# Kernel tuning notes

Hardware: AMD Instinct MI355X
Metric: run time of the kernel (lower is better)

The kernel has to match this reference:

```python
import jax, jax.numpy as jnp
import numpy as np

NUM_TOKENS = 4096
HIDDEN = 2048
INTER = 1408
NUM_EXPERTS = 8
TOP_K = 2


def setup_inputs() -> dict:
    key = jax.random.key(0)
    k1, k2, k3, k4, k5 = jax.random.split(key, 5)
    hidden_states = jax.random.normal(k1, (NUM_TOKENS, HIDDEN), dtype=jnp.float32)
    # w1: (E, 2*I, H) gate+up fused; w2: (E, H, I)
    w1 = jax.random.normal(k2, (NUM_EXPERTS, 2 * INTER, HIDDEN), dtype=jnp.float32) * (1.0 / np.sqrt(HIDDEN))
    w2 = jax.random.normal(k3, (NUM_EXPERTS, HIDDEN, INTER), dtype=jnp.float32) * (1.0 / np.sqrt(INTER))
    raw = jax.random.uniform(k4, (NUM_TOKENS, TOP_K), dtype=jnp.float32)
    topk_weights = raw / jnp.sum(raw, axis=-1, keepdims=True)  # router softmax-normalized weights
    topk_ids = jax.random.randint(k5, (NUM_TOKENS, TOP_K), 0, NUM_EXPERTS, dtype=jnp.int32)
    return {"hidden_states": hidden_states, "w1": w1, "w2": w2,
            "topk_weights": topk_weights, "topk_ids": topk_ids}


def reference(hidden_states, w1, w2, topk_weights, topk_ids):
    """Math-equivalent of fused_experts (dispatch -> grouped gate_up GEMM ->
    SwiGLU -> grouped down GEMM -> weighted scatter-combine).

    Expressed densely per expert (E is small and fixed), which yields the
    identical output to the sorted/grouped-GEMM formulation.
    """
    E = w1.shape[0]
    inter = w1.shape[1] // 2
    dtype = hidden_states.dtype
    # gate_up projection for every expert: [E, N, 2I]
    gate_up = jnp.einsum('nh,eih->eni', hidden_states, w1)
    gate, up = gate_up[..., :inter], gate_up[..., inter:]
    act = jax.nn.silu(gate) * up  # npu_swiglu: silu(first half) * second half
    # down projection: [E, N, H]
    expert_out = jnp.einsum('eni,ehi->enh', act, w2)
    # combine weight per (token, expert): sum of topk_weights where routed
    one_hot = jax.nn.one_hot(topk_ids, E, dtype=dtype)          # [N, K, E]
    combine = jnp.sum(topk_weights[:, :, None] * one_hot, axis=1)  # [N, E]
    return jnp.einsum('ne,enh->nh', combine, expert_out)
```

## Files before the change

kernel.cpp:

```cpp
#include <hip/hip_runtime.h>
#include <hip/hip_bf16.h>

#define NTOK 4096
#define HID 2048
#define INTER 1408
#define NEXP 8
#define NPAIR 8192
#define NKT1 32
#define NK2 44
#define G2SZ 24576

typedef short bf16x8 __attribute__((ext_vector_type(8)));
typedef float f32x4 __attribute__((ext_vector_type(4)));

__device__ __forceinline__ unsigned short f2bf(float f) {
  unsigned u = __builtin_bit_cast(unsigned, f);
  u += 0x7fffu + ((u >> 16) & 1u);
  return (unsigned short)(u >> 16);
}
__device__ __forceinline__ float bf2f(unsigned short v) {
  return __builtin_bit_cast(float, (unsigned)v << 16);
}

__device__ __forceinline__ void gload16(const void* g, void* l) {
  __builtin_amdgcn_global_load_lds(
      (const __attribute__((address_space(1))) void*)g,
      (__attribute__((address_space(3))) void*)l, 16, 0, 0);
}

__device__ __forceinline__ int xcd_swz(int lin, int nwg) {
  int xcd = lin & 7, base = lin >> 3;
  int q = nwg >> 3, r = nwg & 7;
  return (xcd < r ? xcd * (q + 1) : r * (q + 1) + (xcd - r) * q) + base;
}

#define BAR __builtin_amdgcn_s_barrier()
#define SCHED0 __builtin_amdgcn_sched_barrier(0)
#define LGKM0 asm volatile("s_waitcnt lgkmcnt(0)" ::: "memory")
#define VM6 asm volatile("s_waitcnt vmcnt(6)" ::: "memory")
#define VM3 asm volatile("s_waitcnt vmcnt(3)" ::: "memory")
#define VM0 asm volatile("s_waitcnt vmcnt(0)" ::: "memory")
#define PRIO1 __builtin_amdgcn_s_setprio(1)
#define PRIO0 __builtin_amdgcn_s_setprio(0)

__global__ void k_prep(const float* __restrict__ hs, const float* __restrict__ w1,
                       unsigned short* __restrict__ dst,
                       const int* __restrict__ ids, int* __restrict__ ctrl,
                       unsigned short* __restrict__ row_token,
                       unsigned short* __restrict__ inv_row) {
  if (blockIdx.x == 0) {
    __shared__ int cnt[NEXP], cur[NEXP];
    int t = threadIdx.x;
    if (t < NEXP) cnt[t] = 0;
    __syncthreads();
    for (int p = t; p < NPAIR; p += 512) atomicAdd(&cnt[ids[p]], 1);
    __syncthreads();
    if (t == 0) {
      int acc = 0, T1 = 0, T2 = 0;
      for (int e = 0; e < NEXP; ++e) {
        cur[e] = acc;
        ctrl[e] = cnt[e];
        ctrl[8 + e] = acc;
        int n1 = (cnt[e] + 255) >> 8;
        for (int m = 0; m < n1; ++m) { ctrl[32 + T1] = e; ctrl[72 + T1] = m; ++T1; }
        int n2 = (cnt[e] + 127) >> 7;
        for (int m = 0; m < n2; ++m) { ctrl[112 + T2] = e; ctrl[184 + T2] = m; ++T2; }
        acc += cnt[e];
      }
      ctrl[16] = T1;
      ctrl[17] = T2;
    }
    __syncthreads();
    for (int p = t; p < NPAIR; p += 512) {
      int e = ids[p];
      int pos = atomicAdd(&cur[e], 1);
      row_token[pos] = (unsigned short)(p >> 1);
      inv_row[p] = (unsigned short)pos;
    }
    return;
  }
  const int N0 = NTOK * HID / 4;
  const int N1 = N0 + NEXP * 2 * INTER * HID / 4;
  int stride = (gridDim.x - 1) * 512;
  for (int i = (blockIdx.x - 1) * 512 + threadIdx.x; i < N1; i += stride) {
    const float* s = (i < N0) ? hs : w1;
    int o = (i < N0) ? i : i - N0;
    float4 v = reinterpret_cast<const float4*>(s)[o];
    ushort4 u;
    u.x = f2bf(v.x); u.y = f2bf(v.y); u.z = f2bf(v.z); u.w = f2bf(v.w);
    reinterpret_cast<ushort4*>(dst)[i] = u;
  }
}


#define G1_STAGE_A(BB, u, ktile) \
  gload16(asrc[(u)*2+0] + (ktile)*64, lds + (BB) + ((u)*2+0)*4096 + wvb); \
  gload16(asrc[(u)*2+1] + (ktile)*64, lds + (BB) + ((u)*2+1)*4096 + wvb);
#define G1_STAGE_B(BB, u, ktile) \
  gload16(bsrc[(u)*2+0] + (ktile)*64, lds + (BB) + 16384 + ((u)*2+0)*4096 + wvb); \
  gload16(bsrc[(u)*2+1] + (ktile)*64, lds + (BB) + 16384 + ((u)*2+1)*4096 + wvb);

#define G1_READ_A(dst, BB, mh) \
  _Pragma("unroll") for (int m_ = 0; m_ < 4; ++m_) { \
    dst[m_][0] = *(const bf16x8*)(lds + (BB) + aoff + (mh)*8192 + m_*1024 + csw0); \
    dst[m_][1] = *(const bf16x8*)(lds + (BB) + aoff + (mh)*8192 + m_*1024 + csw1); \
  }
#define G1_READ_B(dst, BB, nh) \
  _Pragma("unroll") for (int n_ = 0; n_ < 2; ++n_) { \
    dst[n_][0] = *(const bf16x8*)(lds + (BB) + boff + (nh)*8192 + n_*1024 + csw0); \
    dst[n_][1] = *(const bf16x8*)(lds + (BB) + boff + (nh)*8192 + n_*1024 + csw1); \
  }

#define G1_MMA_Q(afr, bfr, mh, nh) \
  _Pragma("unroll") for (int m_ = 0; m_ < 4; ++m_) \
  _Pragma("unroll") for (int n_ = 0; n_ < 2; ++n_) { \
    acc[(mh)*4+m_][(nh)*2+n_] = __builtin_amdgcn_mfma_f32_16x16x32_bf16(afr[m_][0], bfr[n_][0], acc[(mh)*4+m_][(nh)*2+n_], 0, 0, 0); \
    acc[(mh)*4+m_][(nh)*2+n_] = __builtin_amdgcn_mfma_f32_16x16x32_bf16(afr[m_][1], bfr[n_][1], acc[(mh)*4+m_][(nh)*2+n_], 0, 0, 0); \
  }

#define G1_EIGHT(kt) \
  G1_READ_A(afM0, 0, 0) G1_READ_B(bfN0, 0, 0) G1_STAGE_B(32768, 1, (kt)+1); \
  BAR; LGKM0; PRIO1; G1_MMA_Q(afM0, bfN0, 0, 0) PRIO0; BAR; \
  G1_READ_B(bfN1, 0, 1) G1_STAGE_B(0, 0, (kt)+2); \
  BAR; LGKM0; PRIO1; G1_MMA_Q(afM0, bfN1, 0, 1) PRIO0; BAR; \
  G1_READ_A(afM1, 0, 1) G1_STAGE_A(0, 0, (kt)+2); \
  BAR; LGKM0; PRIO1; G1_MMA_Q(afM1, bfN1, 1, 1) PRIO0; BAR; \
  G1_STAGE_A(0, 1, (kt)+2); \
  BAR; LGKM0; PRIO1; G1_MMA_Q(afM1, bfN0, 1, 0) PRIO0; VM6; BAR; \
  G1_READ_A(afM0, 32768, 0) G1_READ_B(bfN0, 32768, 0) G1_STAGE_B(0, 1, (kt)+2); \
  BAR; LGKM0; PRIO1; G1_MMA_Q(afM0, bfN0, 0, 0) PRIO0; BAR; \
  G1_READ_B(bfN1, 32768, 1) G1_STAGE_B(32768, 0, (kt)+3); \
  BAR; LGKM0; PRIO1; G1_MMA_Q(afM0, bfN1, 0, 1) PRIO0; BAR; \
  G1_READ_A(afM1, 32768, 1) G1_STAGE_A(32768, 0, (kt)+3); \
  BAR; LGKM0; PRIO1; G1_MMA_Q(afM1, bfN1, 1, 1) PRIO0; BAR; \
  G1_STAGE_A(32768, 1, (kt)+3); \
  BAR; LGKM0; PRIO1; G1_MMA_Q(afM1, bfN0, 1, 0) PRIO0; VM6; BAR;

#define G1_EPI(kt) \
  G1_READ_A(afM0, 0, 0) G1_READ_B(bfN0, 0, 0) G1_STAGE_B(32768, 1, (kt)+1); \
  BAR; LGKM0; PRIO1; G1_MMA_Q(afM0, bfN0, 0, 0) PRIO0; BAR; \
  G1_READ_B(bfN1, 0, 1) \
  BAR; LGKM0; PRIO1; G1_MMA_Q(afM0, bfN1, 0, 1) PRIO0; BAR; \
  G1_READ_A(afM1, 0, 1) \
  BAR; LGKM0; PRIO1; G1_MMA_Q(afM1, bfN1, 1, 1) PRIO0; BAR; \
  BAR; LGKM0; PRIO1; G1_MMA_Q(afM1, bfN0, 1, 0) PRIO0; VM0; BAR; \
  G1_READ_A(afM0, 32768, 0) G1_READ_B(bfN0, 32768, 0) \
  BAR; LGKM0; PRIO1; G1_MMA_Q(afM0, bfN0, 0, 0) PRIO0; BAR; \
  G1_READ_B(bfN1, 32768, 1) \
  BAR; LGKM0; PRIO1; G1_MMA_Q(afM0, bfN1, 0, 1) PRIO0; BAR; \
  G1_READ_A(afM1, 32768, 1) \
  BAR; LGKM0; PRIO1; G1_MMA_Q(afM1, bfN1, 1, 1) PRIO0; BAR; \
  LGKM0; PRIO1; G1_MMA_Q(afM1, bfN0, 1, 0) PRIO0;

__global__ __launch_bounds__(512, 2) void k_gemm1(
    const unsigned short* __restrict__ hs,
    const unsigned short* __restrict__ w1,
    const float* __restrict__ w2f,
    unsigned short* __restrict__ w2b,
    const int* __restrict__ ctrl,
    const unsigned short* __restrict__ row_token,
    unsigned short* __restrict__ act) {
  const int T1 = ctrl[16];
  const int nwg = T1 * 11;
  const int lin = blockIdx.x;
  if (lin >= nwg) {
    const int NW2 = NEXP * HID * INTER / 4;
    int nc = gridDim.x - nwg;
    for (int i = (lin - nwg) * 512 + threadIdx.x; i < NW2; i += nc * 512) {
      float4 v = reinterpret_cast<const float4*>(w2f)[i];
      ushort4 u;
      u.x = f2bf(v.x); u.y = f2bf(v.y); u.z = f2bf(v.z); u.w = f2bf(v.w);
      reinterpret_cast<ushort4*>(w2b)[i] = u;
    }
    return;
  }
  const int wg = xcd_swz(lin, nwg);
  const int ti = wg / 11;
  const int nt = wg - ti * 11;
  const int e = ctrl[32 + ti], mt = ctrl[72 + ti];
  const int rows = ctrl[e], off_e = ctrl[8 + e];
  const int n0g = nt * 128;
  const unsigned short* w1e = w1 + (size_t)e * (2 * INTER * HID);

  __shared__ unsigned short smem[65536];
  unsigned short* lds = smem;

  const int t = threadIdx.x;
  const int lane = t & 63, wv = t >> 6;
  const int wm = wv >> 2, wn = wv & 3;
  const int lm = lane & 15, hi4 = lane >> 4;
  const int wvb = (t & 448) * 8;
  const int aoff = (wm * 64 + lm) * 64;
  const int boff = 16384 + (wn * 32 + lm) * 64;
  const int csw0 = (hi4 ^ (lm & 7)) * 8;
  const int csw1 = ((4 + hi4) ^ (lm & 7)) * 8;

  const unsigned short* asrc[4];
#pragma unroll
  for (int i = 0; i < 4; ++i) {
    int p = i * 64 + (t >> 3);
    int r = ((p >> 6) & 1) * 128 + (p >> 7) * 64 + (p & 63);
    int grow = mt * 256 + r;
    if (grow > rows - 1) grow = rows - 1;
    int token = row_token[off_e + grow];
    asrc[i] = hs + (size_t)token * HID + ((t & 7) ^ (p & 7)) * 8;
  }
  const unsigned short* bsrc[4];
#pragma unroll
  for (int i = 0; i < 4; ++i) {
    int p = i * 64 + (t >> 3);
    int nh = p >> 7, wns = (p & 127) >> 5, idx = p & 31;
    int c = n0g + wns * 32 + idx + nh * INTER;
    bsrc[i] = w1e + (size_t)c * HID + ((t & 7) ^ (p & 7)) * 8;
  }

  f32x4 acc[8][4];
#pragma unroll
  for (int i = 0; i < 8; ++i)
#pragma unroll
    for (int j = 0; j < 4; ++j) acc[i][j] = (f32x4){0.f, 0.f, 0.f, 0.f};
  bf16x8 afM0[4][2], afM1[4][2], bfN0[2][2], bfN1[2][2];

  G1_STAGE_B(0, 0, 0) G1_STAGE_A(0, 0, 0) G1_STAGE_A(0, 1, 0) G1_STAGE_B(0, 1, 0)
  G1_STAGE_B(32768, 0, 1) G1_STAGE_A(32768, 0, 1) G1_STAGE_A(32768, 1, 1)
  VM6; BAR;

  for (int kt = 0; kt + 3 < NKT1; kt += 2) { G1_EIGHT(kt) }
  G1_EPI(NKT1 - 2)

#pragma unroll
  for (int mh = 0; mh < 2; ++mh)
#pragma unroll
    for (int m = 0; m < 4; ++m)
#pragma unroll
      for (int n = 0; n < 2; ++n) {
        int col = n0g + wn * 32 + n * 16 + lm;
#pragma unroll
        for (int j = 0; j < 4; ++j) {
          int grow = mt * 256 + wm * 128 + mh * 64 + m * 16 + hi4 * 4 + j;
          if (grow < rows) {
            float g = acc[mh * 4 + m][n][j];
            float u = acc[mh * 4 + m][2 + n][j];
            float a = g / (1.0f + __expf(-g)) * u;
            act[(size_t)(off_e + grow) * INTER + col] = f2bf(a);
          }
        }
      }
}

#define T_STAGE(BB, kt) { \
  gload16(aptr + (size_t)(kt)*32, smem + (BB) + wvb16); \
  gload16(bptr0 + (size_t)(kt)*32, smem + (BB) + 8192 + wvb16); \
  gload16(bptr1 + (size_t)(kt)*32, smem + (BB) + 16384 + wvb16); }

#define T_RD(BB) { \
  _Pragma("unroll") for (int m_ = 0; m_ < 4; ++m_) \
    af[m_] = *(const bf16x8*)(smem + (BB) + arow + m_*1024 + swz); \
  _Pragma("unroll") for (int n_ = 0; n_ < 2; ++n_) { \
    b0[n_] = *(const bf16x8*)(smem + (BB) + brow + n_*1024 + swz); \
    b1[n_] = *(const bf16x8*)(smem + (BB) + brow + 8192 + n_*1024 + swz); } }

#define T_MMA \
  _Pragma("unroll") for (int m_ = 0; m_ < 4; ++m_) \
  _Pragma("unroll") for (int n_ = 0; n_ < 2; ++n_) { \
    acc0[m_][n_] = __builtin_amdgcn_mfma_f32_16x16x32_bf16(af[m_], b0[n_], acc0[m_][n_], 0, 0, 0); \
    acc1[m_][n_] = __builtin_amdgcn_mfma_f32_16x16x32_bf16(af[m_], b1[n_], acc1[m_][n_], 0, 0, 0); }

__global__ __launch_bounds__(512, 4) void k_gemm2(
    const unsigned short* __restrict__ act,
    const unsigned short* __restrict__ w2,
    const int* __restrict__ ctrl,
    unsigned short* __restrict__ eo) {
  const int T2 = ctrl[17];
  const int nwg = T2 * 8;
  const int lin = blockIdx.x;
  if (lin >= nwg) return;
  const int wg = xcd_swz(lin, nwg);
  const int ti = wg >> 3;
  const int nt = wg & 7;
  const int e = ctrl[112 + ti], mt = ctrl[184 + ti];
  const int rows = ctrl[e], off_e = ctrl[8 + e];
  const int n0 = nt * 256;
  const unsigned short* w2e = w2 + (size_t)e * (HID * INTER);

  __shared__ __align__(16) char smem[2 * G2SZ];

  const int t = threadIdx.x;
  const int lane = t & 63, wv = t >> 6;
  const int wm = wv >> 2, wn = wv & 3;
  const int lm = lane & 15, hi4 = lane >> 4;
  const int wvb16 = (t & 448) * 16;
  const int arow = wm * 4096 + lm * 64;
  const int brow = 8192 + wn * 2048 + lm * 64;
  const int swz = (hi4 ^ ((lm >> 1) & 3)) * 16;

  const unsigned short *aptr, *bptr0, *bptr1;
  {
    int cl8 = ((t & 3) ^ ((t >> 3) & 3)) * 8;
    int r = t >> 2;
    int g0 = mt * 128 + r; if (g0 > rows - 1) g0 = rows - 1;
    aptr = act + (size_t)(off_e + g0) * INTER + cl8;
    bptr0 = w2e + (size_t)(n0 + r) * INTER + cl8;
    bptr1 = w2e + (size_t)(n0 + 128 + r) * INTER + cl8;
  }

  f32x4 acc0[4][2], acc1[4][2];
#pragma unroll
  for (int m = 0; m < 4; ++m)
#pragma unroll
    for (int n = 0; n < 2; ++n) {
      acc0[m][n] = (f32x4){0.f, 0.f, 0.f, 0.f};
      acc1[m][n] = (f32x4){0.f, 0.f, 0.f, 0.f};
    }
  bf16x8 af[4], b0[2], b1[2];

  T_STAGE(0, 0)
  T_STAGE(G2SZ, 1)
  VM3; BAR;
  unsigned cur = 0, oth = G2SZ;
  for (int kt = 0; kt < NK2; ++kt) {
    T_RD(cur)
    LGKM0; BAR;
    SCHED0;
    if (kt + 2 < NK2) { T_STAGE(cur, kt + 2) }
    PRIO1; T_MMA PRIO0;
    if (kt < NK2 - 2) { VM3; BAR; }
    else if (kt == NK2 - 2) { VM0; BAR; }
    unsigned tmp = cur; cur = oth; oth = tmp;
  }

#pragma unroll
  for (int m = 0; m < 4; ++m)
#pragma unroll
    for (int n = 0; n < 2; ++n) {
      int col = n0 + wn * 32 + n * 16 + lm;
#pragma unroll
      for (int j = 0; j < 4; ++j) {
        int grow = mt * 128 + wm * 64 + m * 16 + hi4 * 4 + j;
        if (grow < rows) {
          size_t base = (size_t)(off_e + grow) * HID;
          eo[base + col] = f2bf(acc0[m][n][j]);
          eo[base + col + 128] = f2bf(acc1[m][n][j]);
        }
      }
    }
}

__global__ void k_combine(const unsigned short* __restrict__ eo,
                          const float* __restrict__ tw,
                          const unsigned short* __restrict__ inv_row,
                          float* __restrict__ out) {
  int idx = blockIdx.x * blockDim.x + threadIdx.x;
  int tok = idx >> 8;
  int c8 = (idx & 255) * 8;
  int r0 = inv_row[tok * 2], r1 = inv_row[tok * 2 + 1];
  float w0 = tw[tok * 2], w1 = tw[tok * 2 + 1];
  bf16x8 v0 = *(const bf16x8*)(eo + (size_t)r0 * HID + c8);
  bf16x8 v1 = *(const bf16x8*)(eo + (size_t)r1 * HID + c8);
  float4 o0, o1;
  o0.x = w0 * bf2f((unsigned short)v0[0]) + w1 * bf2f((unsigned short)v1[0]);
  o0.y = w0 * bf2f((unsigned short)v0[1]) + w1 * bf2f((unsigned short)v1[1]);
  o0.z = w0 * bf2f((unsigned short)v0[2]) + w1 * bf2f((unsigned short)v1[2]);
  o0.w = w0 * bf2f((unsigned short)v0[3]) + w1 * bf2f((unsigned short)v1[3]);
  o1.x = w0 * bf2f((unsigned short)v0[4]) + w1 * bf2f((unsigned short)v1[4]);
  o1.y = w0 * bf2f((unsigned short)v0[5]) + w1 * bf2f((unsigned short)v1[5]);
  o1.z = w0 * bf2f((unsigned short)v0[6]) + w1 * bf2f((unsigned short)v1[6]);
  o1.w = w0 * bf2f((unsigned short)v0[7]) + w1 * bf2f((unsigned short)v1[7]);
  float4* op = reinterpret_cast<float4*>(out) + (size_t)tok * 512 + (idx & 255) * 2;
  op[0] = o0;
  op[1] = o1;
}

extern "C" void kernel_launch(void* const* d_in, const int* in_sizes, int n_in,
                              void* d_out, int out_size, void* d_ws, size_t ws_size,
                              hipStream_t stream) {
  const float* hs_f = (const float*)d_in[0];
  const float* w1_f = (const float*)d_in[1];
  const float* w2_f = (const float*)d_in[2];
  const float* tw   = (const float*)d_in[3];
  const int*   tids = (const int*)d_in[4];
  float* out = (float*)d_out;

  char* ws = (char*)d_ws;
  unsigned short* hs_b = (unsigned short*)(ws);
  unsigned short* w1_b = (unsigned short*)(ws + 16777216);
  unsigned short* w2_b = (unsigned short*)(ws + 109051904);
  unsigned short* act  = (unsigned short*)(ws + 155189248);
  unsigned short* eo   = (unsigned short*)(ws + 16777216);
  int* ctrl = (int*)(ws + 178257920);
  unsigned short* row_token = (unsigned short*)(ws + 178258944);
  unsigned short* inv_row   = (unsigned short*)(ws + 178275328);

  k_prep<<<2049, 512, 0, stream>>>(hs_f, w1_f, hs_b, tids, ctrl, row_token, inv_row);

  k_gemm1<<<1024, 512, 0, stream>>>(hs_b, w1_b, w2_f, w2_b, ctrl, row_token, act);
  k_gemm2<<<72 * 8, 512, 0, stream>>>(act, w2_b, ctrl, eo);
  k_combine<<<NTOK * HID / 8 / 256, 256, 0, stream>>>(eo, tw, inv_row, out);
}
```

Measured before the change: 257.8 us.

## Fuse fp32-to-bf16 conversion of activations and w1 into gate_up GEMM loads

```diff
diff --git a/kernel.cpp b/kernel.cpp
--- a/kernel.cpp
+++ b/kernel.cpp
@@ -6,12 +6,14 @@
 #define INTER 1408
 #define NEXP 8
 #define NPAIR 8192
-#define NKT1 32
+#define NK1 64
 #define NK2 44
+#define G1B 32768
 #define G2SZ 24576
 
 typedef short bf16x8 __attribute__((ext_vector_type(8)));
 typedef float f32x4 __attribute__((ext_vector_type(4)));
+typedef unsigned u32x4 __attribute__((ext_vector_type(4)));
 
 __device__ __forceinline__ unsigned short f2bf(float f) {
   unsigned u = __builtin_bit_cast(unsigned, f);
@@ -21,6 +23,13 @@
 __device__ __forceinline__ float bf2f(unsigned short v) {
   return __builtin_bit_cast(float, (unsigned)v << 16);
 }
+__device__ __forceinline__ unsigned pk2(float lo, float hi) {
+  return (unsigned)f2bf(lo) | ((unsigned)f2bf(hi) << 16);
+}
+__device__ __forceinline__ bf16x8 cvt8(float4 a, float4 b) {
+  u32x4 u = { pk2(a.x, a.y), pk2(a.z, a.w), pk2(b.x, b.y), pk2(b.z, b.w) };
+  return __builtin_bit_cast(bf16x8, u);
+}
 
 __device__ __forceinline__ void gload16(const void* g, void* l) {
   __builtin_amdgcn_global_load_lds(
@@ -37,124 +46,81 @@
 #define BAR __builtin_amdgcn_s_barrier()
 #define SCHED0 __builtin_amdgcn_sched_barrier(0)
 #define LGKM0 asm volatile("s_waitcnt lgkmcnt(0)" ::: "memory")
-#define VM6 asm volatile("s_waitcnt vmcnt(6)" ::: "memory")
 #define VM3 asm volatile("s_waitcnt vmcnt(3)" ::: "memory")
 #define VM0 asm volatile("s_waitcnt vmcnt(0)" ::: "memory")
 #define PRIO1 __builtin_amdgcn_s_setprio(1)
 #define PRIO0 __builtin_amdgcn_s_setprio(0)
 
-__global__ void k_prep(const float* __restrict__ hs, const float* __restrict__ w1,
-                       unsigned short* __restrict__ dst,
-                       const int* __restrict__ ids, int* __restrict__ ctrl,
-                       unsigned short* __restrict__ row_token,
-                       unsigned short* __restrict__ inv_row) {
-  if (blockIdx.x == 0) {
-    __shared__ int cnt[NEXP], cur[NEXP];
-    int t = threadIdx.x;
-    if (t < NEXP) cnt[t] = 0;
-    __syncthreads();
-    for (int p = t; p < NPAIR; p += 512) atomicAdd(&cnt[ids[p]], 1);
-    __syncthreads();
-    if (t == 0) {
-      int acc = 0, T1 = 0, T2 = 0;
-      for (int e = 0; e < NEXP; ++e) {
-        cur[e] = acc;
-        ctrl[e] = cnt[e];
-        ctrl[8 + e] = acc;
-        int n1 = (cnt[e] + 255) >> 8;
-        for (int m = 0; m < n1; ++m) { ctrl[32 + T1] = e; ctrl[72 + T1] = m; ++T1; }
-        int n2 = (cnt[e] + 127) >> 7;
-        for (int m = 0; m < n2; ++m) { ctrl[112 + T2] = e; ctrl[184 + T2] = m; ++T2; }
-        acc += cnt[e];
-      }
-      ctrl[16] = T1;
-      ctrl[17] = T2;
+__global__ void k_route(const int* __restrict__ ids, int* __restrict__ ctrl,
+                        unsigned short* __restrict__ row_token,
+                        unsigned short* __restrict__ inv_row) {
+  __shared__ int cnt[NEXP], cur[NEXP];
+  int t = threadIdx.x;
+  if (t < NEXP) cnt[t] = 0;
+  __syncthreads();
+  for (int p = t; p < NPAIR; p += 512) atomicAdd(&cnt[ids[p]], 1);
+  __syncthreads();
+  if (t == 0) {
+    int acc = 0, T1 = 0, T2 = 0;
+    for (int e = 0; e < NEXP; ++e) {
+      cur[e] = acc;
+      ctrl[e] = cnt[e];
+      ctrl[8 + e] = acc;
+      int n1 = (cnt[e] + 255) >> 8;
+      for (int m = 0; m < n1; ++m) { ctrl[32 + T1] = e; ctrl[72 + T1] = m; ++T1; }
+      int n2 = (cnt[e] + 127) >> 7;
+      for (int m = 0; m < n2; ++m) { ctrl[112 + T2] = e; ctrl[184 + T2] = m; ++T2; }
+      acc += cnt[e];
     }
-    __syncthreads();
-    for (int p = t; p < NPAIR; p += 512) {
-      int e = ids[p];
-      int pos = atomicAdd(&cur[e], 1);
-      row_token[pos] = (unsigned short)(p >> 1);
-      inv_row[p] = (unsigned short)pos;
-    }
-    return;
-  }
-  const int N0 = NTOK * HID / 4;
-  const int N1 = N0 + NEXP * 2 * INTER * HID / 4;
-  int stride = (gridDim.x - 1) * 512;
-  for (int i = (blockIdx.x - 1) * 512 + threadIdx.x; i < N1; i += stride) {
-    const float* s = (i < N0) ? hs : w1;
-    int o = (i < N0) ? i : i - N0;
-    float4 v = reinterpret_cast<const float4*>(s)[o];
-    ushort4 u;
-    u.x = f2bf(v.x); u.y = f2bf(v.y); u.z = f2bf(v.z); u.w = f2bf(v.w);
-    reinterpret_cast<ushort4*>(dst)[i] = u;
-  }
-}
-
-
-#define G1_STAGE_A(BB, u, ktile) \
-  gload16(asrc[(u)*2+0] + (ktile)*64, lds + (BB) + ((u)*2+0)*4096 + wvb); \
-  gload16(asrc[(u)*2+1] + (ktile)*64, lds + (BB) + ((u)*2+1)*4096 + wvb);
-#define G1_STAGE_B(BB, u, ktile) \
-  gload16(bsrc[(u)*2+0] + (ktile)*64, lds + (BB) + 16384 + ((u)*2+0)*4096 + wvb); \
-  gload16(bsrc[(u)*2+1] + (ktile)*64, lds + (BB) + 16384 + ((u)*2+1)*4096 + wvb);
-
-#define G1_READ_A(dst, BB, mh) \
-  _Pragma("unroll") for (int m_ = 0; m_ < 4; ++m_) { \
-    dst[m_][0] = *(const bf16x8*)(lds + (BB) + aoff + (mh)*8192 + m_*1024 + csw0); \
-    dst[m_][1] = *(const bf16x8*)(lds + (BB) + aoff + (mh)*8192 + m_*1024 + csw1); \
-  }
-#define G1_READ_B(dst, BB, nh) \
-  _Pragma("unroll") for (int n_ = 0; n_ < 2; ++n_) { \
-    dst[n_][0] = *(const bf16x8*)(lds + (BB) + boff + (nh)*8192 + n_*1024 + csw0); \
-    dst[n_][1] = *(const bf16x8*)(lds + (BB) + boff + (nh)*8192 + n_*1024 + csw1); \
-  }
-
-#define G1_MMA_Q(afr, bfr, mh, nh) \
-  _Pragma("unroll") for (int m_ = 0; m_ < 4; ++m_) \
-  _Pragma("unroll") for (int n_ = 0; n_ < 2; ++n_) { \
-    acc[(mh)*4+m_][(nh)*2+n_] = __builtin_amdgcn_mfma_f32_16x16x32_bf16(afr[m_][0], bfr[n_][0], acc[(mh)*4+m_][(nh)*2+n_], 0, 0, 0); \
-    acc[(mh)*4+m_][(nh)*2+n_] = __builtin_amdgcn_mfma_f32_16x16x32_bf16(afr[m_][1], bfr[n_][1], acc[(mh)*4+m_][(nh)*2+n_], 0, 0, 0); \
-  }
-
-#define G1_EIGHT(kt) \
-  G1_READ_A(afM0, 0, 0) G1_READ_B(bfN0, 0, 0) G1_STAGE_B(32768, 1, (kt)+1); \
-  BAR; LGKM0; PRIO1; G1_MMA_Q(afM0, bfN0, 0, 0) PRIO0; BAR; \
-  G1_READ_B(bfN1, 0, 1) G1_STAGE_B(0, 0, (kt)+2); \
-  BAR; LGKM0; PRIO1; G1_MMA_Q(afM0, bfN1, 0, 1) PRIO0; BAR; \
-  G1_READ_A(afM1, 0, 1) G1_STAGE_A(0, 0, (kt)+2); \
-  BAR; LGKM0; PRIO1; G1_MMA_Q(afM1, bfN1, 1, 1) PRIO0; BAR; \
-  G1_STAGE_A(0, 1, (kt)+2); \
-  BAR; LGKM0; PRIO1; G1_MMA_Q(afM1, bfN0, 1, 0) PRIO0; VM6; BAR; \
-  G1_READ_A(afM0, 32768, 0) G1_READ_B(bfN0, 32768, 0) G1_STAGE_B(0, 1, (kt)+2); \
-  BAR; LGKM0; PRIO1; G1_MMA_Q(afM0, bfN0, 0, 0) PRIO0; BAR; \
-  G1_READ_B(bfN1, 32768, 1) G1_STAGE_B(32768, 0, (kt)+3); \
-  BAR; LGKM0; PRIO1; G1_MMA_Q(afM0, bfN1, 0, 1) PRIO0; BAR; \
-  G1_READ_A(afM1, 32768, 1) G1_STAGE_A(32768, 0, (kt)+3); \
-  BAR; LGKM0; PRIO1; G1_MMA_Q(afM1, bfN1, 1, 1) PRIO0; BAR; \
-  G1_STAGE_A(32768, 1, (kt)+3); \
-  BAR; LGKM0; PRIO1; G1_MMA_Q(afM1, bfN0, 1, 0) PRIO0; VM6; BAR;
-
-#define G1_EPI(kt) \
-  G1_READ_A(afM0, 0, 0) G1_READ_B(bfN0, 0, 0) G1_STAGE_B(32768, 1, (kt)+1); \
-  BAR; LGKM0; PRIO1; G1_MMA_Q(afM0, bfN0, 0, 0) PRIO0; BAR; \
-  G1_READ_B(bfN1, 0, 1) \
-  BAR; LGKM0; PRIO1; G1_MMA_Q(afM0, bfN1, 0, 1) PRIO0; BAR; \
-  G1_READ_A(afM1, 0, 1) \
-  BAR; LGKM0; PRIO1; G1_MMA_Q(afM1, bfN1, 1, 1) PRIO0; BAR; \
-  BAR; LGKM0; PRIO1; G1_MMA_Q(afM1, bfN0, 1, 0) PRIO0; VM0; BAR; \
-  G1_READ_A(afM0, 32768, 0) G1_READ_B(bfN0, 32768, 0) \
-  BAR; LGKM0; PRIO1; G1_MMA_Q(afM0, bfN0, 0, 0) PRIO0; BAR; \
-  G1_READ_B(bfN1, 32768, 1) \
-  BAR; LGKM0; PRIO1; G1_MMA_Q(afM0, bfN1, 0, 1) PRIO0; BAR; \
-  G1_READ_A(afM1, 32768, 1) \
-  BAR; LGKM0; PRIO1; G1_MMA_Q(afM1, bfN1, 1, 1) PRIO0; BAR; \
-  LGKM0; PRIO1; G1_MMA_Q(afM1, bfN0, 1, 0) PRIO0;
+    ctrl[16] = T1;
+    ctrl[17] = T2;
+  }
+  __syncthreads();
+  for (int p = t; p < NPAIR; p += 512) {
+    int e = ids[p];
+    int pos = atomicAdd(&cur[e], 1);
+    row_token[pos] = (unsigned short)(p >> 1);
+    inv_row[p] = (unsigned short)pos;
+  }
+}
+
+
+#define G1_LOAD(F, P, kt) { \
+  const float* p_ = (P) + (size_t)(kt) * 32; \
+  F[0] = *(const float4*)(p_ + c0); F[1] = *(const float4*)(p_ + c0 + 4); \
+  F[2] = *(const float4*)(p_ + c1); F[3] = *(const float4*)(p_ + c1 + 4); }
+
+#define G1_WRA(BB, F) { \
+  *(bf16x8*)(smem + (BB) + wdA)      = cvt8(F[0], F[1]); \
+  *(bf16x8*)(smem + (BB) + wdA + 16) = cvt8(F[2], F[3]); }
+#define G1_WRB(BB, F) { \
+  *(bf16x8*)(smem + (BB) + wdB)      = cvt8(F[0], F[1]); \
+  *(bf16x8*)(smem + (BB) + wdB + 16) = cvt8(F[2], F[3]); }
+
+#define G1_RDLO(BB) { \
+  _Pragma("unroll") for (int m_ = 0; m_ < 4; ++m_) \
+    af[m_] = *(const bf16x8*)(smem + (BB) + aoff + m_*1024 + swz); \
+  _Pragma("unroll") for (int n_ = 0; n_ < 2; ++n_) { \
+    bg[n_] = *(const bf16x8*)(smem + (BB) + bgoff + n_*1024 + swz); \
+    bu[n_] = *(const bf16x8*)(smem + (BB) + buoff + n_*1024 + swz); } }
+#define G1_RDHI(BB) { \
+  _Pragma("unroll") for (int m_ = 0; m_ < 4; ++m_) \
+    af[m_] = *(const bf16x8*)(smem + (BB) + aoff + 4096 + m_*1024 + swz); }
+
+#define G1_MMALO \
+  _Pragma("unroll") for (int m_ = 0; m_ < 4; ++m_) \
+  _Pragma("unroll") for (int n_ = 0; n_ < 2; ++n_) { \
+    acc[m_][n_]     = __builtin_amdgcn_mfma_f32_16x16x32_bf16(af[m_], bg[n_], acc[m_][n_], 0, 0, 0); \
+    acc[m_][2 + n_] = __builtin_amdgcn_mfma_f32_16x16x32_bf16(af[m_], bu[n_], acc[m_][2 + n_], 0, 0, 0); }
+#define G1_MMAHI \
+  _Pragma("unroll") for (int m_ = 0; m_ < 4; ++m_) \
+  _Pragma("unroll") for (int n_ = 0; n_ < 2; ++n_) { \
+    acc[4 + m_][n_]     = __builtin_amdgcn_mfma_f32_16x16x32_bf16(af[m_], bg[n_], acc[4 + m_][n_], 0, 0, 0); \
+    acc[4 + m_][2 + n_] = __builtin_amdgcn_mfma_f32_16x16x32_bf16(af[m_], bu[n_], acc[4 + m_][2 + n_], 0, 0, 0); }
 
 __global__ __launch_bounds__(512, 2) void k_gemm1(
-    const unsigned short* __restrict__ hs,
-    const unsigned short* __restrict__ w1,
+    const float* __restrict__ hsF,
+    const float* __restrict__ w1F,
     const float* __restrict__ w2f,
     unsigned short* __restrict__ w2b,
     const int* __restrict__ ctrl,
@@ -180,38 +146,36 @@
   const int e = ctrl[32 + ti], mt = ctrl[72 + ti];
   const int rows = ctrl[e], off_e = ctrl[8 + e];
   const int n0g = nt * 128;
-  const unsigned short* w1e = w1 + (size_t)e * (2 * INTER * HID);
-
-  __shared__ unsigned short smem[65536];
-  unsigned short* lds = smem;
+  const float* w1e = w1F + (size_t)e * (2 * INTER * HID);
+
+  __shared__ __align__(16) char smem[2 * G1B];
 
   const int t = threadIdx.x;
   const int lane = t & 63, wv = t >> 6;
   const int wm = wv >> 2, wn = wv & 3;
   const int lm = lane & 15, hi4 = lane >> 4;
-  const int wvb = (t & 448) * 8;
-  const int aoff = (wm * 64 + lm) * 64;
-  const int boff = 16384 + (wn * 32 + lm) * 64;
-  const int csw0 = (hi4 ^ (lm & 7)) * 8;
-  const int csw1 = ((4 + hi4) ^ (lm & 7)) * 8;
-
-  const unsigned short* asrc[4];
-#pragma unroll
-  for (int i = 0; i < 4; ++i) {
-    int p = i * 64 + (t >> 3);
-    int r = ((p >> 6) & 1) * 128 + (p >> 7) * 64 + (p & 63);
+  const int swz = (hi4 ^ ((lm >> 1) & 3)) * 16;
+  const int aoff = wm * 8192 + lm * 64;
+  const int bgoff = 16384 + wn * 2048 + lm * 64;
+  const int buoff = 24576 + wn * 2048 + lm * 64;
+
+  const int r = t >> 1, h = t & 1;
+  const int s4 = (t >> 2) & 3;
+  const int c0 = ((2 * h) ^ s4) * 8;
+  const int c1 = ((2 * h + 1) ^ s4) * 8;
+  const int wdA = r * 64 + h * 32;
+  const int wdB = 16384 + r * 64 + h * 32;
+
+  const float* aP;
+  {
     int grow = mt * 256 + r;
     if (grow > rows - 1) grow = rows - 1;
-    int token = row_token[off_e + grow];
-    asrc[i] = hs + (size_t)token * HID + ((t & 7) ^ (p & 7)) * 8;
-  }
-  const unsigned short* bsrc[4];
-#pragma unroll
-  for (int i = 0; i < 4; ++i) {
-    int p = i * 64 + (t >> 3);
-    int nh = p >> 7, wns = (p & 127) >> 5, idx = p & 31;
-    int c = n0g + wns * 32 + idx + nh * INTER;
-    bsrc[i] = w1e + (size_t)c * HID + ((t & 7) ^ (p & 7)) * 8;
+    aP = hsF + (size_t)row_token[off_e + grow] * HID;
+  }
+  const float* bP;
+  {
+    int cg = (r < 128) ? (n0g + r) : (INTER + n0g + (r - 128));
+    bP = w1e + (size_t)cg * HID;
   }
 
   f32x4 acc[8][4];
@@ -219,14 +183,40 @@
   for (int i = 0; i < 8; ++i)
 #pragma unroll
     for (int j = 0; j < 4; ++j) acc[i][j] = (f32x4){0.f, 0.f, 0.f, 0.f};
-  bf16x8 afM0[4][2], afM1[4][2], bfN0[2][2], bfN1[2][2];
-
-  G1_STAGE_B(0, 0, 0) G1_STAGE_A(0, 0, 0) G1_STAGE_A(0, 1, 0) G1_STAGE_B(0, 1, 0)
-  G1_STAGE_B(32768, 0, 1) G1_STAGE_A(32768, 0, 1) G1_STAGE_A(32768, 1, 1)
-  VM6; BAR;
-
-  for (int kt = 0; kt + 3 < NKT1; kt += 2) { G1_EIGHT(kt) }
-  G1_EPI(NKT1 - 2)
+  bf16x8 af[4], bg[2], bu[2];
+  float4 fA0[4], fB0[4], fA1[4], fB1[4];
+
+  G1_LOAD(fA0, aP, 0) G1_LOAD(fB0, bP, 0)
+  G1_LOAD(fA1, aP, 1) G1_LOAD(fB1, bP, 1)
+  G1_WRA(0, fA0) G1_WRB(0, fB0)
+  LGKM0; BAR;
+
+  for (int kt = 0; kt < NK1; kt += 2) {
+    const bool l2 = (kt + 2) < NK1, l3 = (kt + 3) < NK1;
+    G1_RDLO(0)
+    G1_WRA(G1B, fA1)
+    if (l2) { G1_LOAD(fA0, aP, kt + 2) }
+    LGKM0; BAR;
+    PRIO1; G1_MMALO PRIO0;
+
+    G1_RDHI(0)
+    G1_WRB(G1B, fB1)
+    if (l2) { G1_LOAD(fB0, bP, kt + 2) }
+    LGKM0; BAR;
+    PRIO1; G1_MMAHI PRIO0;
+
+    G1_RDLO(G1B)
+    if (l2) { G1_WRA(0, fA0) }
+    if (l3) { G1_LOAD(fA1, aP, kt + 3) }
+    LGKM0; BAR;
+    PRIO1; G1_MMALO PRIO0;
+
+    G1_RDHI(G1B)
+    if (l2) { G1_WRB(0, fB0) }
+    if (l3) { G1_LOAD(fB1, bP, kt + 3) }
+    LGKM0; BAR;
+    PRIO1; G1_MMAHI PRIO0;
+  }
 
 #pragma unroll
   for (int mh = 0; mh < 2; ++mh)
@@ -382,8 +372,6 @@
   float* out = (float*)d_out;
 
   char* ws = (char*)d_ws;
-  unsigned short* hs_b = (unsigned short*)(ws);
-  unsigned short* w1_b = (unsigned short*)(ws + 16777216);
   unsigned short* w2_b = (unsigned short*)(ws + 109051904);
   unsigned short* act  = (unsigned short*)(ws + 155189248);
   unsigned short* eo   = (unsigned short*)(ws + 16777216);
@@ -391,9 +379,9 @@
   unsigned short* row_token = (unsigned short*)(ws + 178258944);
   unsigned short* inv_row   = (unsigned short*)(ws + 178275328);
 
-  k_prep<<<2049, 512, 0, stream>>>(hs_f, w1_f, hs_b, tids, ctrl, row_token, inv_row);
-
-  k_gemm1<<<1024, 512, 0, stream>>>(hs_b, w1_b, w2_f, w2_b, ctrl, row_token, act);
+  k_route<<<1, 512, 0, stream>>>(tids, ctrl, row_token, inv_row);
+
+  k_gemm1<<<1024, 512, 0, stream>>>(hs_f, w1_f, w2_f, w2_b, ctrl, row_token, act);
   k_gemm2<<<72 * 8, 512, 0, stream>>>(act, w2_b, ctrl, eo);
   k_combine<<<NTOK * HID / 8 / 256, 256, 0, stream>>>(eo, tw, inv_row, out);
 }
```

New measurement: 591.0 us. 2.29x slower.
